# Optimization experiments

Measured on AMD Instinct MI355X. Metric: run time of the kernel, lower is better.

Reference implementation:

```python
import jax, jax.numpy as jnp
import numpy as np

B, S, D, H = 2, 4096, 512, 8
HD = D // H  # head_dim = 64


def setup_inputs() -> dict:
    key = jax.random.key(0)
    ks = jax.random.split(key, 13)
    scale = 1.0 / np.sqrt(D)
    inp = {
        "query": jax.random.normal(ks[0], (B, S, D), dtype=jnp.float32),
        "key": jax.random.normal(ks[1], (B, S, D), dtype=jnp.float32),
        "value": jax.random.normal(ks[2], (B, S, D), dtype=jnp.float32),
        "mask": jax.random.randint(ks[3], (B, S, S), 0, 2, dtype=jnp.int32),
        "Wq": jax.random.normal(ks[4], (D, D), dtype=jnp.float32) * scale,
        "bq": jnp.zeros((D,), dtype=jnp.float32),
        "Wk": jax.random.normal(ks[5], (D, D), dtype=jnp.float32) * scale,
        "bk": jnp.zeros((D,), dtype=jnp.float32),
        "Wv": jax.random.normal(ks[6], (D, D), dtype=jnp.float32) * scale,
        "bv": jnp.zeros((D,), dtype=jnp.float32),
        "Wo": jax.random.normal(ks[7], (D, D), dtype=jnp.float32) * scale,
        "bo": jnp.zeros((D,), dtype=jnp.float32),
    }
    return inp


def reference(query, key, value, mask, Wq, bq, Wk, bk, Wv, bv, Wo, bo):
    # Linear projections (torch Linear: x @ W.T + b), split heads: [B,H,S,HD]
    def split_heads(x):
        return x.reshape(B, S, H, HD).transpose(0, 2, 1, 3)

    q = split_heads(query @ Wq.T + bq)
    k = split_heads(key @ Wk.T + bk)
    v = split_heads(value @ Wv.T + bv)

    # NOTE: original module applies NO 1/sqrt(head_dim) scaling.
    scores = jnp.einsum("bhqd,bhkd->bhqk", q, k)  # [B,H,S,S]
    scores = jnp.where(mask[:, None, :, :] == 0, jnp.float32(-1e9), scores)
    probs = jax.nn.softmax(scores, axis=-1)
    attn = jnp.einsum("bhqk,bhkd->bhqd", probs, v)  # [B,H,S,HD]
    attn = attn.transpose(0, 2, 1, 3).reshape(B, S, D)
    return attn @ Wo.T + bo
```

## Files before the change

### kernel.cpp

```cpp
#include <hip/hip_runtime.h>
#include <hip/hip_bf16.h>
#include <cstddef>
#include <cstdint>


#define S_LEN 4096
#define DMODEL 512
#define NHEAD 8
#define HDIM 64
#define NWORDS (S_LEN / 64)

typedef __bf16 bf16x8 __attribute__((ext_vector_type(8)));
typedef _Float16 f16x8 __attribute__((ext_vector_type(8)));
typedef float f32x4 __attribute__((ext_vector_type(4)));
typedef float f32x16 __attribute__((ext_vector_type(16)));
typedef int i32x2 __attribute__((ext_vector_type(2)));
typedef unsigned int u32x4 __attribute__((ext_vector_type(4)));
typedef unsigned short u16x4 __attribute__((ext_vector_type(4)));
typedef unsigned short u16x8 __attribute__((ext_vector_type(8)));

__device__ __forceinline__ unsigned short f2bf(float x) {
  return __builtin_bit_cast(unsigned short, (__bf16)x);
}
__device__ __forceinline__ float bf2f(unsigned short h) {
  union { unsigned u; float f; } v; v.u = ((unsigned)h) << 16; return v.f;
}
__device__ __forceinline__ float fast_exp2(float x) {
#if __has_builtin(__builtin_amdgcn_exp2f)
  return __builtin_amdgcn_exp2f(x);
#else
  return __expf(x * 0.69314718056f);
#endif
}
__device__ __forceinline__ float max3f(float a, float b, float c) {
  return fmaxf(fmaxf(a, b), c);
}
__device__ __forceinline__ int bit_mask(unsigned hs, int bs) {
#if __has_builtin(__builtin_amdgcn_sbfe)
  return __builtin_amdgcn_sbfe((int)hs, bs, 1);
#else
  return ((int)(hs << (31 - bs))) >> 31;
#endif
}
__device__ __forceinline__ float mask_blend(float x, int msk) {
  const int NEG = __builtin_bit_cast(int, -1.0e9f);
  int xi = __builtin_bit_cast(int, x);
  return __builtin_bit_cast(float, (xi & msk) | (NEG & ~msk));
}
__device__ __forceinline__ void pl_swap(int& a, int& b) {
#if __has_builtin(__builtin_amdgcn_permlane32_swap)
  i32x2 r = __builtin_amdgcn_permlane32_swap(a, b, false, false);
  a = r[0]; b = r[1];
#else
  asm volatile("v_permlane32_swap_b32 %0, %1" : "+v"(a), "+v"(b));
#endif
}
__device__ __forceinline__ float xhalf_max(float x) {
  int a = __builtin_bit_cast(int, x), b = a;
  pl_swap(a, b);
  return fmaxf(__builtin_bit_cast(float, a), __builtin_bit_cast(float, b));
}
__device__ __forceinline__ float xhalf_sum(float x) {
  int a = __builtin_bit_cast(int, x), b = a;
  pl_swap(a, b);
  return __builtin_bit_cast(float, a) + __builtin_bit_cast(float, b);
}
__device__ __forceinline__ int swzi(int row, int col) {
  return row * 64 + ((col & 7) | ((((col >> 3) ^ row) & 7) << 3));
}

__global__ __launch_bounds__(256) void prep(
    const float* __restrict__ query, const float* __restrict__ key,
    const float* __restrict__ value,
    const float* __restrict__ w0, const float* __restrict__ w1,
    const float* __restrict__ w2, const float* __restrict__ w3,
    const int* __restrict__ mask,
    unsigned short* __restrict__ qh, unsigned short* __restrict__ ql,
    unsigned short* __restrict__ kh, unsigned short* __restrict__ kl,
    unsigned short* __restrict__ vh, unsigned short* __restrict__ vl,
    unsigned short* __restrict__ wbuf, unsigned long long* __restrict__ bits)
{
  const int task = blockIdx.y;
  const int tid = blockIdx.x * 256 + threadIdx.x;
  const int nthr = gridDim.x * 256;

  if (task < 3) {
    const float* x = (task == 0) ? query : (task == 1) ? key : value;
    unsigned short* h = (task == 0) ? qh : (task == 1) ? kh : vh;
    unsigned short* l = (task == 0) ? ql : (task == 1) ? kl : vl;
    const int n4 = (int)((size_t)2 * S_LEN * DMODEL / 4);
    for (int i = tid; i < n4; i += nthr) {
      float4 f = ((const float4*)x)[i];
      float ff[4] = {f.x, f.y, f.z, f.w};
      u16x4 hh, ll;
      #pragma unroll
      for (int j = 0; j < 4; ++j) {
        unsigned short hb = f2bf(ff[j]);
        hh[j] = hb;
        ll[j] = f2bf(ff[j] - bf2f(hb));
      }
      ((u16x4*)h)[i] = hh;
      ((u16x4*)l)[i] = ll;
    }
  } else if (task == 3) {
    const int per = 65536;
    for (int i = tid; i < 4 * per; i += nthr) {
      int wsel = i >> 16, idx = i & (per - 1);
      const float* src = (wsel == 0) ? w0 : (wsel == 1) ? w1 : (wsel == 2) ? w2 : w3;
      unsigned short* h = wbuf + (size_t)wsel * 2 * 262144;
      unsigned short* l = h + 262144;
      float4 f = ((const float4*)src)[idx];
      float ff[4] = {f.x, f.y, f.z, f.w};
      u16x4 hh, ll;
      #pragma unroll
      for (int j = 0; j < 4; ++j) {
        unsigned short hb = f2bf(ff[j]);
        hh[j] = hb;
        ll[j] = f2bf(ff[j] - bf2f(hb));
      }
      ((u16x4*)h)[idx] = hh;
      ((u16x4*)l)[idx] = ll;
    }
  } else {
    const int nwords = 2 * S_LEN * NWORDS;
    int gw = tid >> 6;
    int lane = threadIdx.x & 63;
    int nw = nthr >> 6;
    for (int w = gw; w < nwords; w += nw) {
      int v = mask[(size_t)w * 64 + lane];
      unsigned long long bm = __ballot(v != 0);
      if (lane == 0) bits[w] = bm;
    }
  }
}

template <int MODE>
__global__ __launch_bounds__(256) void gemm_pre(
    const unsigned short* __restrict__ xh, const unsigned short* __restrict__ xl,
    const unsigned short* __restrict__ wh, const unsigned short* __restrict__ wl,
    const float* __restrict__ bias, void* __restrict__ out0, float oscale)
{
  constexpr bool TRI = (MODE == 0);
  __shared__ __align__(16) unsigned short SMEM[24576];
  unsigned short* Xh = SMEM;
  unsigned short* Xl = SMEM + 8192;
  unsigned short* Wh = SMEM + 16384;
  unsigned short* Wl = SMEM + 20480;

  const int t = threadIdx.x;
  const int lane = t & 63;
  const int w = t >> 6;
  const int c = lane & 15;
  const int g = lane >> 4;
  const int row0 = blockIdx.x * 128;
  const int col0 = blockIdx.y * 64;

  f32x4 acc[2][4];
  #pragma unroll
  for (int mi = 0; mi < 2; ++mi)
    #pragma unroll
    for (int n = 0; n < 4; ++n) acc[mi][n] = (f32x4){0.f, 0.f, 0.f, 0.f};

  u16x8 pxh[4], pxl[4], pwh[2], pwl[2];
  auto issue = [&](int k0) {
    #pragma unroll
    for (int i = 0; i < 4; ++i) {
      int id = i * 256 + t;
      int r = id >> 3, ch = id & 7;
      size_t off = (size_t)(row0 + r) * DMODEL + k0 + ch * 8;
      pxh[i] = *(const u16x8*)(xh + off);
      if (TRI) pxl[i] = *(const u16x8*)(xl + off);
    }
    #pragma unroll
    for (int i = 0; i < 2; ++i) {
      int id = i * 256 + t;
      int r = id >> 3, ch = id & 7;
      size_t off = (size_t)(col0 + r) * DMODEL + k0 + ch * 8;
      pwh[i] = *(const u16x8*)(wh + off);
      if (TRI) pwl[i] = *(const u16x8*)(wl + off);
    }
  };
  auto commit = [&]() {
    #pragma unroll
    for (int i = 0; i < 4; ++i) {
      int id = i * 256 + t;
      int r = id >> 3, ch = id & 7;
      int dst = r * 64 + (((ch ^ r) & 7) << 3);
      *(u16x8*)&Xh[dst] = pxh[i];
      if (TRI) *(u16x8*)&Xl[dst] = pxl[i];
    }
    #pragma unroll
    for (int i = 0; i < 2; ++i) {
      int id = i * 256 + t;
      int r = id >> 3, ch = id & 7;
      int dst = r * 64 + (((ch ^ r) & 7) << 3);
      *(u16x8*)&Wh[dst] = pwh[i];
      if (TRI) *(u16x8*)&Wl[dst] = pwl[i];
    }
  };

  issue(0);
  commit();
  __syncthreads();

  for (int k0 = 0; k0 < DMODEL; k0 += 64) {
    const bool more = (k0 + 64) < DMODEL;
    if (more) issue(k0 + 64);

    #pragma unroll
    for (int kk = 0; kk < 2; ++kk) {
      bf16x8 ah[2], al[2], bh_[4], bl_[4];
      #pragma unroll
      for (int mi = 0; mi < 2; ++mi) {
        int r = w * 32 + mi * 16 + c;
        ah[mi] = __builtin_bit_cast(bf16x8, *(const u16x8*)&Xh[swzi(r, (kk * 4 + g) * 8)]);
        if (TRI) al[mi] = __builtin_bit_cast(bf16x8, *(const u16x8*)&Xl[swzi(r, (kk * 4 + g) * 8)]);
      }
      #pragma unroll
      for (int n = 0; n < 4; ++n) {
        int r = n * 16 + c;
        bh_[n] = __builtin_bit_cast(bf16x8, *(const u16x8*)&Wh[swzi(r, (kk * 4 + g) * 8)]);
        if (TRI) bl_[n] = __builtin_bit_cast(bf16x8, *(const u16x8*)&Wl[swzi(r, (kk * 4 + g) * 8)]);
      }
      #pragma unroll
      for (int mi = 0; mi < 2; ++mi)
        #pragma unroll
        for (int n = 0; n < 4; ++n) {
          acc[mi][n] = __builtin_amdgcn_mfma_f32_16x16x32_bf16(ah[mi], bh_[n], acc[mi][n], 0, 0, 0);
          if (TRI) {
            acc[mi][n] = __builtin_amdgcn_mfma_f32_16x16x32_bf16(al[mi], bh_[n], acc[mi][n], 0, 0, 0);
            acc[mi][n] = __builtin_amdgcn_mfma_f32_16x16x32_bf16(ah[mi], bl_[n], acc[mi][n], 0, 0, 0);
          }
        }
    }
    __syncthreads();
    if (more) {
      commit();
      __syncthreads();
    }
  }

  if (MODE == 0) {
    unsigned short* Yf = (unsigned short*)out0;
    #pragma unroll
    for (int mi = 0; mi < 2; ++mi)
      #pragma unroll
      for (int n = 0; n < 4; ++n)
        #pragma unroll
        for (int j = 0; j < 4; ++j) {
          int rr = row0 + w * 32 + mi * 16 + g * 4 + j;
          int oo = col0 + n * 16 + c;
          float val = (acc[mi][n][j] + bias[oo]) * oscale;
          int bb = rr >> 12, ss = rr & (S_LEN - 1), h2 = oo >> 6, hd = oo & 63;
          size_t idx = (((size_t)(bb * NHEAD + h2)) * S_LEN + ss) * HDIM + hd;
          Yf[idx] = __builtin_bit_cast(unsigned short, (_Float16)val);
        }
  } else if (MODE == 1) {
    float* Y = (float*)out0;
    #pragma unroll
    for (int mi = 0; mi < 2; ++mi)
      #pragma unroll
      for (int n = 0; n < 4; ++n)
        #pragma unroll
        for (int j = 0; j < 4; ++j) {
          int rr = row0 + w * 32 + mi * 16 + g * 4 + j;
          int oo = col0 + n * 16 + c;
          Y[(size_t)rr * DMODEL + oo] = acc[mi][n][j] + bias[oo];
        }
  } else {
    unsigned short* Ts = SMEM;
    __syncthreads();
    #pragma unroll
    for (int mi = 0; mi < 2; ++mi)
      #pragma unroll
      for (int n = 0; n < 4; ++n)
        #pragma unroll
        for (int j = 0; j < 4; ++j) {
          int r = w * 32 + mi * 16 + g * 4 + j;
          int o = n * 16 + c;
          Ts[r * 68 + o] = __builtin_bit_cast(unsigned short, (_Float16)(acc[mi][n][j] + bias[col0 + o]));
        }
    __syncthreads();
    unsigned short* vt = (unsigned short*)out0;
    int bb = row0 >> 12, sbase = row0 & (S_LEN - 1), h2 = col0 >> 6;
    int d = t >> 2, s0 = (t & 3) * 32;
    size_t obase = ((size_t)((bb * NHEAD + h2) * HDIM + d)) * S_LEN + sbase + s0;
    #pragma unroll
    for (int i = 0; i < 4; ++i) {
      u16x8 v;
      #pragma unroll
      for (int jj = 0; jj < 8; ++jj) v[jj] = Ts[(s0 + i * 8 + jj) * 68 + d];
      *(u16x8*)(vt + obase + i * 8) = v;
    }
  }
}

__global__ __launch_bounds__(256) void attn32(
    const unsigned short* __restrict__ qf, const unsigned short* __restrict__ kf,
    const unsigned short* __restrict__ vt, const unsigned long long* __restrict__ mbits,
    unsigned short* __restrict__ Ob)
{
  __shared__ __align__(16) unsigned short LDS[2][2][4096];

  const int t = threadIdx.x;
  const int lane = t & 63;
  const int w = t >> 6;
  const int pair = w >> 1;
  const int chunk = w & 1;
  const int c31 = lane & 31;
  const int hi = lane >> 5;

  const int nwg = gridDim.x;
  const int bid = blockIdx.x;
  const int lin = (bid & 7) * (nwg >> 3) + (bid >> 3);
  const int qi = lin & 63;
  const int bh = lin >> 6;
  const int q0 = qi * 64;
  const int b = bh >> 3, h = bh & 7;
  const int qrow = q0 + pair * 32 + c31;

  const unsigned short* Qp = qf + ((size_t)bh * S_LEN + qrow) * HDIM;
  f16x8 qfr[4];
  #pragma unroll
  for (int s = 0; s < 4; ++s)
    qfr[s] = __builtin_bit_cast(f16x8, *(const u16x8*)(Qp + 16 * s + 8 * hi));

  const unsigned short* Kb = kf + (size_t)bh * S_LEN * HDIM;
  const unsigned short* Vbt = vt + (size_t)bh * HDIM * S_LEN;
  const unsigned long long* mptr = mbits + (size_t)(b * S_LEN + qrow) * NWORDS;

  const int sr0 = t >> 3, sch = t & 7;
  const int sr1 = sr0 + 32;
  const int dst0 = sr0 * 64 + (((sch ^ sr0) & 7) << 3);
  const int dst1 = sr1 * 64 + (((sch ^ sr1) & 7) << 3);
  u16x8 pkk[2], pkv[2];
  auto issue = [&](int k0) {
    pkk[0] = *(const u16x8*)(Kb + (size_t)(k0 + sr0) * HDIM + sch * 8);
    pkk[1] = *(const u16x8*)(Kb + (size_t)(k0 + sr1) * HDIM + sch * 8);
    pkv[0] = *(const u16x8*)(Vbt + (size_t)sr0 * S_LEN + k0 + sch * 8);
    pkv[1] = *(const u16x8*)(Vbt + (size_t)sr1 * S_LEN + k0 + sch * 8);
  };
  auto commit = [&](int buf) {
    *(u16x8*)&LDS[buf][0][dst0] = pkk[0];
    *(u16x8*)&LDS[buf][0][dst1] = pkk[1];
    *(u16x8*)&LDS[buf][1][dst0] = pkv[0];
    *(u16x8*)&LDS[buf][1][dst1] = pkv[1];
  };

  f32x16 oacc0, oacc1;
  #pragma unroll
  for (int r = 0; r < 16; ++r) { oacc0[r] = 0.f; oacc1[r] = 0.f; }
  const f32x16 fzero = oacc0;
  float mrow = -INFINITY, lrow = 0.f;

  unsigned long long m64 = mptr[0], m64n = 0;

  issue(0);
  commit(0);
  __syncthreads();

  int cur = 0;
  for (int kt = 0; kt < S_LEN / 64; ++kt) {
    const bool more = kt < (S_LEN / 64 - 1);
    if (more) {
      issue((kt + 1) * 64);
      m64n = mptr[kt + 1];
    }
    const unsigned short* K_ = &LDS[cur][0][0];
    const unsigned short* Vt_ = &LDS[cur][1][0];

    f32x16 p;
    __builtin_amdgcn_s_setprio(1);
    {
      int idx = swzi(chunk * 32 + c31, 8 * hi);
      f16x8 kfr = __builtin_bit_cast(f16x8, *(const u16x8*)&K_[idx]);
      p = __builtin_amdgcn_mfma_f32_32x32x16_f16(kfr, qfr[0], fzero, 0, 0, 0);
    }
    #pragma unroll
    for (int s = 1; s < 4; ++s) {
      int idx = swzi(chunk * 32 + c31, 16 * s + 8 * hi);
      f16x8 kfr = __builtin_bit_cast(f16x8, *(const u16x8*)&K_[idx]);
      p = __builtin_amdgcn_mfma_f32_32x32x16_f16(kfr, qfr[s], p, 0, 0, 0);
    }
    __builtin_amdgcn_s_setprio(0);

    unsigned half = chunk ? (unsigned)(m64 >> 32) : (unsigned)m64;
    unsigned hs = half >> (hi * 4);
    #pragma unroll
    for (int r = 0; r < 16; ++r) {
      int bs = (r & 3) + 8 * (r >> 2);
      p[r] = mask_blend(p[r], bit_mask(hs, bs));
    }

    float t0 = max3f(p[0], p[1], p[2]);
    float t1 = max3f(p[3], p[4], p[5]);
    float t2 = max3f(p[6], p[7], p[8]);
    float t3 = max3f(p[9], p[10], p[11]);
    float t4 = max3f(p[12], p[13], p[14]);
    float mx = fmaxf(max3f(t0, t1, t2), max3f(t3, t4, p[15]));
    mx = xhalf_max(mx);

    float mn, scl;
    if (__all(mx <= mrow + 11.54f)) {
      mn = mrow;
      scl = 1.0f;
    } else {
      mn = fmaxf(mrow, mx);
      scl = fast_exp2(mrow - mn);
      mrow = mn;
      oacc0 *= scl;
      oacc1 *= scl;
    }

    #pragma unroll
    for (int r = 0; r < 16; ++r) p[r] = fast_exp2(p[r] - mn);

    float s0_ = (p[0] + p[1]) + (p[2] + p[3]);
    float s1_ = (p[4] + p[5]) + (p[6] + p[7]);
    float s2_ = (p[8] + p[9]) + (p[10] + p[11]);
    float s3_ = (p[12] + p[13]) + (p[14] + p[15]);
    float ps = xhalf_sum((s0_ + s1_) + (s2_ + s3_));
    lrow = lrow * scl + ps;

    unsigned W[4][2];
    #pragma unroll
    for (int rq = 0; rq < 4; ++rq) {
      W[rq][0] = __builtin_bit_cast(unsigned, __builtin_amdgcn_cvt_pkrtz(p[4 * rq + 0], p[4 * rq + 1]));
      W[rq][1] = __builtin_bit_cast(unsigned, __builtin_amdgcn_cvt_pkrtz(p[4 * rq + 2], p[4 * rq + 3]));
    }
    f16x8 pf[2];
    #pragma unroll
    for (int s2 = 0; s2 < 2; ++s2) {
      unsigned keep0 = hi ? W[2 * s2 + 1][0] : W[2 * s2][0];
      unsigned keep1 = hi ? W[2 * s2 + 1][1] : W[2 * s2][1];
      unsigned send0 = hi ? W[2 * s2][0] : W[2 * s2 + 1][0];
      unsigned send1 = hi ? W[2 * s2][1] : W[2 * s2 + 1][1];
      unsigned recv0 = (unsigned)__shfl_xor((int)send0, 32, 64);
      unsigned recv1 = (unsigned)__shfl_xor((int)send1, 32, 64);
      u32x4 fw;
      fw[0] = hi ? recv0 : keep0;
      fw[1] = hi ? recv1 : keep1;
      fw[2] = hi ? keep0 : recv0;
      fw[3] = hi ? keep1 : recv1;
      pf[s2] = __builtin_bit_cast(f16x8, fw);
    }

    __builtin_amdgcn_s_setprio(1);
    #pragma unroll
    for (int s2 = 0; s2 < 2; ++s2) {
      int col = chunk * 32 + 16 * s2 + 8 * hi;
      f16x8 vf0 = __builtin_bit_cast(f16x8, *(const u16x8*)&Vt_[swzi(c31, col)]);
      f16x8 vf1 = __builtin_bit_cast(f16x8, *(const u16x8*)&Vt_[swzi(32 + c31, col)]);
      oacc0 = __builtin_amdgcn_mfma_f32_32x32x16_f16(vf0, pf[s2], oacc0, 0, 0, 0);
      oacc1 = __builtin_amdgcn_mfma_f32_32x32x16_f16(vf1, pf[s2], oacc1, 0, 0, 0);
    }
    __builtin_amdgcn_s_setprio(0);

    if (more) {
      m64 = m64n;
      commit(cur ^ 1);
    }
    __syncthreads();
    cur ^= 1;
  }

  float* mb = (float*)&LDS[0][0][0];
  const int mi = ((pair * 2 + hi) * 32 + c31) * 36;
  if (chunk == 1) {
    #pragma unroll
    for (int q4 = 0; q4 < 4; ++q4) {
      *(f32x4*)&mb[mi + q4 * 4]      = (f32x4){oacc0[q4 * 4], oacc0[q4 * 4 + 1], oacc0[q4 * 4 + 2], oacc0[q4 * 4 + 3]};
      *(f32x4*)&mb[mi + 16 + q4 * 4] = (f32x4){oacc1[q4 * 4], oacc1[q4 * 4 + 1], oacc1[q4 * 4 + 2], oacc1[q4 * 4 + 3]};
    }
    mb[mi + 32] = mrow;
    mb[mi + 33] = lrow;
  }
  __syncthreads();
  if (chunk == 0) {
    float m1 = mb[mi + 32], l1 = mb[mi + 33];
    float mS = fmaxf(mrow, m1);
    float f0 = fast_exp2(mrow - mS), f1 = fast_exp2(m1 - mS);
    float lS = lrow * f0 + l1 * f1;
    float inv = 1.0f / lS;
    size_t obase = ((size_t)b * S_LEN + qrow) * DMODEL + h * HDIM;
    #pragma unroll
    for (int c2 = 0; c2 < 2; ++c2) {
      #pragma unroll
      for (int rq = 0; rq < 4; ++rq) {
        u16x4 hv;
        #pragma unroll
        for (int rb = 0; rb < 4; ++rb) {
          int reg = 4 * rq + rb;
          float o0 = (c2 == 0) ? oacc0[reg] : oacc1[reg];
          float o1 = mb[mi + c2 * 16 + reg];
          hv[rb] = f2bf((o0 * f0 + o1 * f1) * inv);
        }
        *(u16x4*)(Ob + obase + 32 * c2 + 8 * rq + 4 * hi) = hv;
      }
    }
  }
}

extern "C" void kernel_launch(void* const* d_in, const int* in_sizes, int n_in,
                              void* d_out, int out_size, void* d_ws, size_t ws_size,
                              hipStream_t stream) {
  const float* query = (const float*)d_in[0];
  const float* key   = (const float*)d_in[1];
  const float* value = (const float*)d_in[2];
  const int*   mask  = (const int*)  d_in[3];
  const float* Wq = (const float*)d_in[4];
  const float* bq = (const float*)d_in[5];
  const float* Wk = (const float*)d_in[6];
  const float* bk = (const float*)d_in[7];
  const float* Wv = (const float*)d_in[8];
  const float* bv = (const float*)d_in[9];
  const float* Wo = (const float*)d_in[10];
  const float* bo = (const float*)d_in[11];
  float* out = (float*)d_out;

  const size_t PER = (size_t)2 * S_LEN * DMODEL;
  const size_t WSZ = (size_t)DMODEL * DMODEL;

  unsigned short* p = (unsigned short*)d_ws;
  unsigned short* wbuf = p;
  unsigned short* xh = p + 8 * WSZ;
  unsigned short* xl = xh + PER;
  unsigned short* yh = xl + PER;
  unsigned short* yl = yh + PER;
  unsigned short* zh = yl + PER;
  unsigned short* zl = zh + PER;
  unsigned short* qfb = zl + PER;
  unsigned short* kfb = qfb + PER;
  unsigned short* vtb = kfb + PER;

  unsigned short* wqh = wbuf + 0 * 2 * WSZ, *wql = wqh + WSZ;
  unsigned short* wkh = wbuf + 1 * 2 * WSZ, *wkl = wkh + WSZ;
  unsigned short* wvh = wbuf + 2 * 2 * WSZ, *wvl = wvh + WSZ;
  unsigned short* woh = wbuf + 3 * 2 * WSZ;

  unsigned long long* bits = (unsigned long long*)d_out;

  prep<<<dim3(2048, 5), 256, 0, stream>>>(query, key, value, Wq, Wk, Wv, Wo, mask,
                                          xh, xl, yh, yl, zh, zl, wbuf, bits);

  dim3 gg(2 * S_LEN / 128, DMODEL / 64);
  gemm_pre<0><<<gg, 256, 0, stream>>>(xh, xl, wqh, wql, bq, qfb, 1.44269504f);
  gemm_pre<0><<<gg, 256, 0, stream>>>(yh, yl, wkh, wkl, bk, kfb, 1.0f);
  gemm_pre<2><<<gg, 256, 0, stream>>>(zh, zl, wvh, wvl, bv, vtb, 1.0f);

  attn32<<<1024, 256, 0, stream>>>(qfb, kfb, vtb, bits, xh);

  gemm_pre<1><<<gg, 256, 0, stream>>>(xh, nullptr, woh, nullptr, bo, out, 1.0f);
}
```

Before: 257.1 us.

## Merge QKV projections into one launch and use direct global-to-LDS loads in attention

The three Q/K/V projection GEMMs become one kernel launched with a z-dimension that picks the mode at runtime. The output projection moves to its own dedicated kernel. The attention kernel now stages K/V tiles through global_load_lds, writing straight into LDS instead of going through registers and then a separate commit step. This saves two launches and frees the register round trip, but a runtime mode branch in the projection kernel may cost registers or code quality, and the direct loads rely on pre-swizzled source addresses and on the barrier for ordering.

```diff
diff --git a/kernel.cpp b/kernel.cpp
--- a/kernel.cpp
+++ b/kernel.cpp
@@ -67,6 +67,11 @@
 }
 __device__ __forceinline__ int swzi(int row, int col) {
   return row * 64 + ((col & 7) | ((((col >> 3) ^ row) & 7) << 3));
+}
+__device__ __forceinline__ void gload16(const unsigned short* g, unsigned short* lds) {
+  __builtin_amdgcn_global_load_lds(
+      (const __attribute__((address_space(1))) unsigned int*)g,
+      (__attribute__((address_space(3))) unsigned int*)lds, 16, 0, 0);
 }
 
 __global__ __launch_bounds__(256) void prep(
@@ -134,13 +139,25 @@
   }
 }
 
-template <int MODE>
-__global__ __launch_bounds__(256) void gemm_pre(
-    const unsigned short* __restrict__ xh, const unsigned short* __restrict__ xl,
-    const unsigned short* __restrict__ wh, const unsigned short* __restrict__ wl,
-    const float* __restrict__ bias, void* __restrict__ out0, float oscale)
+__global__ __launch_bounds__(256) void proj_qkv(
+    const unsigned short* __restrict__ qxh, const unsigned short* __restrict__ qxl,
+    const unsigned short* __restrict__ kxh, const unsigned short* __restrict__ kxl,
+    const unsigned short* __restrict__ vxh, const unsigned short* __restrict__ vxl,
+    const unsigned short* __restrict__ wbuf,
+    const float* __restrict__ bq, const float* __restrict__ bk, const float* __restrict__ bv,
+    unsigned short* __restrict__ qout, unsigned short* __restrict__ kout,
+    unsigned short* __restrict__ vout)
 {
-  constexpr bool TRI = (MODE == 0);
+  const int mode = blockIdx.z;
+  const bool tri = (mode < 2);
+  const unsigned short* xh = (mode == 0) ? qxh : (mode == 1) ? kxh : vxh;
+  const unsigned short* xl = (mode == 0) ? qxl : (mode == 1) ? kxl : vxl;
+  const unsigned short* wh = wbuf + (size_t)mode * 2 * 262144;
+  const unsigned short* wl = wh + 262144;
+  const float* bias = (mode == 0) ? bq : (mode == 1) ? bk : bv;
+  unsigned short* out = (mode == 0) ? qout : (mode == 1) ? kout : vout;
+  const float oscale = (mode == 0) ? 1.44269504f : 1.0f;
+
   __shared__ __align__(16) unsigned short SMEM[24576];
   unsigned short* Xh = SMEM;
   unsigned short* Xl = SMEM + 8192;
@@ -169,7 +186,7 @@
       int r = id >> 3, ch = id & 7;
       size_t off = (size_t)(row0 + r) * DMODEL + k0 + ch * 8;
       pxh[i] = *(const u16x8*)(xh + off);
-      if (TRI) pxl[i] = *(const u16x8*)(xl + off);
+      if (tri) pxl[i] = *(const u16x8*)(xl + off);
     }
     #pragma unroll
     for (int i = 0; i < 2; ++i) {
@@ -177,7 +194,7 @@
       int r = id >> 3, ch = id & 7;
       size_t off = (size_t)(col0 + r) * DMODEL + k0 + ch * 8;
       pwh[i] = *(const u16x8*)(wh + off);
-      if (TRI) pwl[i] = *(const u16x8*)(wl + off);
+      if (tri) pwl[i] = *(const u16x8*)(wl + off);
     }
   };
   auto commit = [&]() {
@@ -187,7 +204,7 @@
       int r = id >> 3, ch = id & 7;
       int dst = r * 64 + (((ch ^ r) & 7) << 3);
       *(u16x8*)&Xh[dst] = pxh[i];
-      if (TRI) *(u16x8*)&Xl[dst] = pxl[i];
+      if (tri) *(u16x8*)&Xl[dst] = pxl[i];
     }
     #pragma unroll
     for (int i = 0; i < 2; ++i) {
@@ -195,7 +212,7 @@
       int r = id >> 3, ch = id & 7;
       int dst = r * 64 + (((ch ^ r) & 7) << 3);
       *(u16x8*)&Wh[dst] = pwh[i];
-      if (TRI) *(u16x8*)&Wl[dst] = pwl[i];
+      if (tri) *(u16x8*)&Wl[dst] = pwl[i];
     }
   };
 
@@ -214,20 +231,20 @@
       for (int mi = 0; mi < 2; ++mi) {
         int r = w * 32 + mi * 16 + c;
         ah[mi] = __builtin_bit_cast(bf16x8, *(const u16x8*)&Xh[swzi(r, (kk * 4 + g) * 8)]);
-        if (TRI) al[mi] = __builtin_bit_cast(bf16x8, *(const u16x8*)&Xl[swzi(r, (kk * 4 + g) * 8)]);
+        if (tri) al[mi] = __builtin_bit_cast(bf16x8, *(const u16x8*)&Xl[swzi(r, (kk * 4 + g) * 8)]);
       }
       #pragma unroll
       for (int n = 0; n < 4; ++n) {
         int r = n * 16 + c;
         bh_[n] = __builtin_bit_cast(bf16x8, *(const u16x8*)&Wh[swzi(r, (kk * 4 + g) * 8)]);
-        if (TRI) bl_[n] = __builtin_bit_cast(bf16x8, *(const u16x8*)&Wl[swzi(r, (kk * 4 + g) * 8)]);
+        if (tri) bl_[n] = __builtin_bit_cast(bf16x8, *(const u16x8*)&Wl[swzi(r, (kk * 4 + g) * 8)]);
       }
       #pragma unroll
       for (int mi = 0; mi < 2; ++mi)
         #pragma unroll
         for (int n = 0; n < 4; ++n) {
           acc[mi][n] = __builtin_amdgcn_mfma_f32_16x16x32_bf16(ah[mi], bh_[n], acc[mi][n], 0, 0, 0);
-          if (TRI) {
+          if (tri) {
             acc[mi][n] = __builtin_amdgcn_mfma_f32_16x16x32_bf16(al[mi], bh_[n], acc[mi][n], 0, 0, 0);
             acc[mi][n] = __builtin_amdgcn_mfma_f32_16x16x32_bf16(ah[mi], bl_[n], acc[mi][n], 0, 0, 0);
           }
@@ -240,8 +257,7 @@
     }
   }
 
-  if (MODE == 0) {
-    unsigned short* Yf = (unsigned short*)out0;
+  if (mode < 2) {
     #pragma unroll
     for (int mi = 0; mi < 2; ++mi)
       #pragma unroll
@@ -253,19 +269,7 @@
           float val = (acc[mi][n][j] + bias[oo]) * oscale;
           int bb = rr >> 12, ss = rr & (S_LEN - 1), h2 = oo >> 6, hd = oo & 63;
           size_t idx = (((size_t)(bb * NHEAD + h2)) * S_LEN + ss) * HDIM + hd;
-          Yf[idx] = __builtin_bit_cast(unsigned short, (_Float16)val);
-        }
-  } else if (MODE == 1) {
-    float* Y = (float*)out0;
-    #pragma unroll
-    for (int mi = 0; mi < 2; ++mi)
-      #pragma unroll
-      for (int n = 0; n < 4; ++n)
-        #pragma unroll
-        for (int j = 0; j < 4; ++j) {
-          int rr = row0 + w * 32 + mi * 16 + g * 4 + j;
-          int oo = col0 + n * 16 + c;
-          Y[(size_t)rr * DMODEL + oo] = acc[mi][n][j] + bias[oo];
+          out[idx] = __builtin_bit_cast(unsigned short, (_Float16)val);
         }
   } else {
     unsigned short* Ts = SMEM;
@@ -281,7 +285,6 @@
           Ts[r * 68 + o] = __builtin_bit_cast(unsigned short, (_Float16)(acc[mi][n][j] + bias[col0 + o]));
         }
     __syncthreads();
-    unsigned short* vt = (unsigned short*)out0;
     int bb = row0 >> 12, sbase = row0 & (S_LEN - 1), h2 = col0 >> 6;
     int d = t >> 2, s0 = (t & 3) * 32;
     size_t obase = ((size_t)((bb * NHEAD + h2) * HDIM + d)) * S_LEN + sbase + s0;
@@ -290,9 +293,103 @@
       u16x8 v;
       #pragma unroll
       for (int jj = 0; jj < 8; ++jj) v[jj] = Ts[(s0 + i * 8 + jj) * 68 + d];
-      *(u16x8*)(vt + obase + i * 8) = v;
+      *(u16x8*)(out + obase + i * 8) = v;
     }
   }
+}
+
+__global__ __launch_bounds__(256) void gemm_out(
+    const unsigned short* __restrict__ xh, const unsigned short* __restrict__ wh,
+    const float* __restrict__ bias, float* __restrict__ Y)
+{
+  __shared__ __align__(16) unsigned short SMEM[24576];
+  unsigned short* Xh = SMEM;
+  unsigned short* Wh = SMEM + 16384;
+
+  const int t = threadIdx.x;
+  const int lane = t & 63;
+  const int w = t >> 6;
+  const int c = lane & 15;
+  const int g = lane >> 4;
+  const int row0 = blockIdx.x * 128;
+  const int col0 = blockIdx.y * 64;
+
+  f32x4 acc[2][4];
+  #pragma unroll
+  for (int mi = 0; mi < 2; ++mi)
+    #pragma unroll
+    for (int n = 0; n < 4; ++n) acc[mi][n] = (f32x4){0.f, 0.f, 0.f, 0.f};
+
+  u16x8 pxh[4], pwh[2];
+  auto issue = [&](int k0) {
+    #pragma unroll
+    for (int i = 0; i < 4; ++i) {
+      int id = i * 256 + t;
+      int r = id >> 3, ch = id & 7;
+      pxh[i] = *(const u16x8*)(xh + (size_t)(row0 + r) * DMODEL + k0 + ch * 8);
+    }
+    #pragma unroll
+    for (int i = 0; i < 2; ++i) {
+      int id = i * 256 + t;
+      int r = id >> 3, ch = id & 7;
+      pwh[i] = *(const u16x8*)(wh + (size_t)(col0 + r) * DMODEL + k0 + ch * 8);
+    }
+  };
+  auto commit = [&]() {
+    #pragma unroll
+    for (int i = 0; i < 4; ++i) {
+      int id = i * 256 + t;
+      int r = id >> 3, ch = id & 7;
+      *(u16x8*)&Xh[r * 64 + (((ch ^ r) & 7) << 3)] = pxh[i];
+    }
+    #pragma unroll
+    for (int i = 0; i < 2; ++i) {
+      int id = i * 256 + t;
+      int r = id >> 3, ch = id & 7;
+      *(u16x8*)&Wh[r * 64 + (((ch ^ r) & 7) << 3)] = pwh[i];
+    }
+  };
+
+  issue(0);
+  commit();
+  __syncthreads();
+
+  for (int k0 = 0; k0 < DMODEL; k0 += 64) {
+    const bool more = (k0 + 64) < DMODEL;
+    if (more) issue(k0 + 64);
+
+    #pragma unroll
+    for (int kk = 0; kk < 2; ++kk) {
+      bf16x8 ah[2], bh_[4];
+      #pragma unroll
+      for (int mi = 0; mi < 2; ++mi)
+        ah[mi] = __builtin_bit_cast(bf16x8, *(const u16x8*)&Xh[swzi(w * 32 + mi * 16 + c, (kk * 4 + g) * 8)]);
+      #pragma unroll
+      for (int n = 0; n < 4; ++n)
+        bh_[n] = __builtin_bit_cast(bf16x8, *(const u16x8*)&Wh[swzi(n * 16 + c, (kk * 4 + g) * 8)]);
+      #pragma unroll
+      for (int mi = 0; mi < 2; ++mi)
+        #pragma unroll
+        for (int n = 0; n < 4; ++n)
+          acc[mi][n] = __builtin_amdgcn_mfma_f32_16x16x32_bf16(ah[mi], bh_[n], acc[mi][n], 0, 0, 0);
+    }
+    __syncthreads();
+    if (more) {
+      commit();
+      __syncthreads();
+    }
+  }
+
+  #pragma unroll
+  for (int mi = 0; mi < 2; ++mi)
+    #pragma unroll
+    for (int n = 0; n < 4; ++n)
+      #pragma unroll
+      for (int j = 0; j < 4; ++j) {
+        int rr = row0 + w * 32 + mi * 16 + g * 4 + j;
+        int oo = col0 + n * 16 + c;
+        Y[(size_t)rr * DMODEL + oo] = acc[mi][n][j] + bias[oo];
+      }
 }
 
 __global__ __launch_bounds__(256) void attn32(
@@ -329,22 +426,24 @@
   const unsigned short* Vbt = vt + (size_t)bh * HDIM * S_LEN;
   const unsigned long long* mptr = mbits + (size_t)(b * S_LEN + qrow) * NWORDS;
 
-  const int sr0 = t >> 3, sch = t & 7;
-  const int sr1 = sr0 + 32;
-  const int dst0 = sr0 * 64 + (((sch ^ sr0) & 7) << 3);
-  const int dst1 = sr1 * 64 + (((sch ^ sr1) & 7) << 3);
-  u16x8 pkk[2], pkv[2];
-  auto issue = [&](int k0) {
-    pkk[0] = *(const u16x8*)(Kb + (size_t)(k0 + sr0) * HDIM + sch * 8);
-    pkk[1] = *(const u16x8*)(Kb + (size_t)(k0 + sr1) * HDIM + sch * 8);
-    pkv[0] = *(const u16x8*)(Vbt + (size_t)sr0 * S_LEN + k0 + sch * 8);
-    pkv[1] = *(const u16x8*)(Vbt + (size_t)sr1 * S_LEN + k0 + sch * 8);
-  };
-  auto commit = [&](int buf) {
-    *(u16x8*)&LDS[buf][0][dst0] = pkk[0];
-    *(u16x8*)&LDS[buf][0][dst1] = pkk[1];
-    *(u16x8*)&LDS[buf][1][dst0] = pkv[0];
-    *(u16x8*)&LDS[buf][1][dst1] = pkv[1];
+  const int idx0 = (w * 2 + 0) * 64 + lane;
+  const int idx1 = (w * 2 + 1) * 64 + lane;
+  const int r0 = idx0 >> 3, r1 = idx1 >> 3;
+  const int c0 = ((lane & 7) ^ r0) & 7, c1 = ((lane & 7) ^ r1) & 7;
+  const unsigned short* nK0 = Kb + r0 * HDIM + c0 * 8;
+  const unsigned short* nK1 = Kb + r1 * HDIM + c1 * 8;
+  const unsigned short* nV0 = Vbt + (size_t)r0 * S_LEN + c0 * 8;
+  const unsigned short* nV1 = Vbt + (size_t)r1 * S_LEN + c1 * 8;
+  const int ld0 = (w * 2 + 0) * 512;
+  const int ld1 = (w * 2 + 1) * 512;
+
+  auto issue = [&](int buf) {
+    gload16(nK0, &LDS[buf][0][ld0]);
+    gload16(nK1, &LDS[buf][0][ld1]);
+    gload16(nV0, &LDS[buf][1][ld0]);
+    gload16(nV1, &LDS[buf][1][ld1]);
+    nK0 += 64 * HDIM; nK1 += 64 * HDIM;
+    nV0 += 64; nV1 += 64;
   };
 
   f32x16 oacc0, oacc1;
@@ -356,14 +455,13 @@
   unsigned long long m64 = mptr[0], m64n = 0;
 
   issue(0);
-  commit(0);
   __syncthreads();
 
   int cur = 0;
   for (int kt = 0; kt < S_LEN / 64; ++kt) {
     const bool more = kt < (S_LEN / 64 - 1);
     if (more) {
-      issue((kt + 1) * 64);
+      issue(cur ^ 1);
       m64n = mptr[kt + 1];
     }
     const unsigned short* K_ = &LDS[cur][0][0];
@@ -456,10 +554,7 @@
     }
     __builtin_amdgcn_s_setprio(0);
 
-    if (more) {
-      m64 = m64n;
-      commit(cur ^ 1);
-    }
+    if (more) m64 = m64n;
     __syncthreads();
     cur ^= 1;
   }
@@ -533,9 +628,6 @@
   unsigned short* kfb = qfb + PER;
   unsigned short* vtb = kfb + PER;
 
-  unsigned short* wqh = wbuf + 0 * 2 * WSZ, *wql = wqh + WSZ;
-  unsigned short* wkh = wbuf + 1 * 2 * WSZ, *wkl = wkh + WSZ;
-  unsigned short* wvh = wbuf + 2 * 2 * WSZ, *wvl = wvh + WSZ;
   unsigned short* woh = wbuf + 3 * 2 * WSZ;
 
   unsigned long long* bits = (unsigned long long*)d_out;
@@ -543,12 +635,10 @@
   prep<<<dim3(2048, 5), 256, 0, stream>>>(query, key, value, Wq, Wk, Wv, Wo, mask,
                                           xh, xl, yh, yl, zh, zl, wbuf, bits);
 
-  dim3 gg(2 * S_LEN / 128, DMODEL / 64);
-  gemm_pre<0><<<gg, 256, 0, stream>>>(xh, xl, wqh, wql, bq, qfb, 1.44269504f);
-  gemm_pre<0><<<gg, 256, 0, stream>>>(yh, yl, wkh, wkl, bk, kfb, 1.0f);
-  gemm_pre<2><<<gg, 256, 0, stream>>>(zh, zl, wvh, wvl, bv, vtb, 1.0f);
+  proj_qkv<<<dim3(2 * S_LEN / 128, DMODEL / 64, 3), 256, 0, stream>>>(
+      xh, xl, yh, yl, zh, zl, wbuf, bq, bk, bv, qfb, kfb, vtb);
 
   attn32<<<1024, 256, 0, stream>>>(qfb, kfb, vtb, bits, xh);
 
-  gemm_pre<1><<<gg, 256, 0, stream>>>(xh, nullptr, woh, nullptr, bo, out, 1.0f);
-}
+  gemm_out<<<dim3(2 * S_LEN / 128, DMODEL / 64), 256, 0, stream>>>(xh, woh, bo, out);
+}
```

Result: faster. 245.7 us, median of 2 (-4.4%).
